# Optimization experiments

Hardware: AMD Instinct MI355X
Metric: run time of the kernel (lower is better)

## Reference

```python
import jax, jax.numpy as jnp
import numpy as np


def setup_inputs() -> dict:
    key = jax.random.key(0)
    ks = jax.random.split(key, 7)
    B, C, W, H = 4, 256, 128, 128
    s = 1.0 / np.sqrt(C)
    return {
        "x": jax.random.normal(ks[0], (B, C, W, H), dtype=jnp.float32),
        "wq": jax.random.normal(ks[1], (C, C), dtype=jnp.float32) * s,
        "bq": jax.random.normal(ks[2], (C,), dtype=jnp.float32) * s,
        "wk": jax.random.normal(ks[3], (C, C), dtype=jnp.float32) * s,
        "bk": jax.random.normal(ks[4], (C,), dtype=jnp.float32) * s,
        "wv": jax.random.normal(ks[5], (C, C), dtype=jnp.float32) * s,
        "bv": jax.random.normal(ks[6], (C,), dtype=jnp.float32) * s,
    }


def reference(x, wq, bq, wk, bk, wv, bv):
    B, C, W, H = x.shape
    N = W * H
    xf = x.reshape(B, C, N)  # flatten spatial: (B, C, N)
    # 1x1 convs are channel-mixing GEMMs: out[b,o,n] = sum_c w[o,c] x[b,c,n] + b[o]
    q = jnp.einsum('oc,bcn->bon', wq, xf) + bq[:, None]
    k = jnp.einsum('oc,bcn->bon', wk, xf) + bk[:, None]
    v = jnp.einsum('oc,bcn->bon', wv, xf) + bv[:, None]
    # channel-channel energy: (B, C, C)
    energy = jnp.einsum('bcn,bdn->bcd', q, k) / jnp.sqrt(jnp.float32(N))
    attention = jax.nn.softmax(energy, axis=-1)
    out = jnp.einsum('bcd,bdn->bcn', attention, v)
    return out.reshape(B, C, W, H) + x
```

## Files before the change

### kernel.cpp

```cpp
#include <hip/hip_runtime.h>
#include <stdint.h>

#define BB 4
#define CC 256
#define NN 16384
#define NSL 32

typedef unsigned short u16;
typedef __attribute__((ext_vector_type(8))) __bf16 bf16x8;
typedef __attribute__((ext_vector_type(4))) float f32x4;

__device__ __forceinline__ u16 f2bf(float f) {
  union { float f; uint32_t u; } c;
  c.f = f;
  uint32_t u = c.u;
  return (u16)((u + 0x7fffu + ((u >> 16) & 1u)) >> 16);
}

__device__ __forceinline__ void g2l16(const u16* g, u16* l) {
  __builtin_amdgcn_global_load_lds((__attribute__((address_space(1))) void*)g,
                                   (__attribute__((address_space(3))) void*)l, 16, 0, 0);
}

__device__ __forceinline__ void stage128x32(const u16* src, int stride, u16* lds, int tid) {
  int r = tid >> 2;
  int c = (tid & 3) << 3;
  g2l16(src + (size_t)r * stride + c, lds + r * 32 + c);
  g2l16(src + (size_t)(r + 64) * stride + c, lds + (r + 64) * 32 + c);
}

__device__ __forceinline__ void stage128x32_w8(const u16* src, int stride, u16* lds, int tid) {
  int r = tid >> 2;
  int c = (tid & 3) << 3;
  g2l16(src + (size_t)r * stride + c, lds + r * 32 + c);
}

__device__ __forceinline__ void stage256x32_w8(const u16* src, int stride, u16* lds, int tid) {
  int r = tid >> 2;
  int c = (tid & 3) << 3;
  g2l16(src + (size_t)r * stride + c, lds + r * 32 + c);
  g2l16(src + (size_t)(r + 128) * stride + c, lds + (r + 128) * 32 + c);
}

__device__ __forceinline__ void mfma_tile(const u16* As, const u16* Bs, int mb, int nb,
                                          int l16, int q8, f32x4 acc[4][4]) {
  bf16x8 af[4], bf[4];
#pragma unroll
  for (int i = 0; i < 4; i++) af[i] = *(const bf16x8*)&As[(mb + i * 16 + l16) * 32 + q8];
#pragma unroll
  for (int i = 0; i < 4; i++) bf[i] = *(const bf16x8*)&Bs[(nb + i * 16 + l16) * 32 + q8];
#pragma unroll
  for (int i = 0; i < 4; i++)
#pragma unroll
    for (int j = 0; j < 4; j++)
      acc[i][j] = __builtin_amdgcn_mfma_f32_16x16x32_bf16(af[i], bf[j], acc[i][j], 0, 0, 0);
}

__global__ __launch_bounds__(256) void prep_kernel(const float* __restrict__ x,
                                                   u16* __restrict__ xb,
                                                   u16* __restrict__ xbT,
                                                   float* __restrict__ s_part) {
  __shared__ float t[64][65];
  __shared__ float rs[64][4];
  int n0 = blockIdx.x * 64, c0 = blockIdx.y * 64, bz = blockIdx.z;
  int tid = threadIdx.x;
  int rr0 = tid >> 4, q4 = (tid & 15) * 4;
  const float* xs = x + ((size_t)bz * CC + c0) * NN + n0;
  u16* xbp = xb + ((size_t)bz * CC + c0) * NN + n0;
#pragma unroll
  for (int cc = rr0; cc < 64; cc += 16) {
    float4 v = *(const float4*)&xs[(size_t)cc * NN + q4];
    t[cc][q4] = v.x; t[cc][q4 + 1] = v.y; t[cc][q4 + 2] = v.z; t[cc][q4 + 3] = v.w;
    union { u16 h[4]; uint2 u; } pk;
    pk.h[0] = f2bf(v.x); pk.h[1] = f2bf(v.y); pk.h[2] = f2bf(v.z); pk.h[3] = f2bf(v.w);
    *(uint2*)&xbp[(size_t)cc * NN + q4] = pk.u;
  }
  __syncthreads();
  {
    int r = tid >> 2, q = tid & 3;
    float p = 0.f;
#pragma unroll
    for (int i = 0; i < 16; i++) p += t[r][q * 16 + i];
    rs[r][q] = p;
  }
  u16* od = xbT + ((size_t)bz * NN + n0) * CC + c0;
#pragma unroll
  for (int nn = rr0; nn < 64; nn += 16) {
    union { u16 h[4]; uint2 u; } pk;
    pk.h[0] = f2bf(t[q4][nn]); pk.h[1] = f2bf(t[q4 + 1][nn]);
    pk.h[2] = f2bf(t[q4 + 2][nn]); pk.h[3] = f2bf(t[q4 + 3][nn]);
    *(uint2*)&od[(size_t)nn * CC + q4] = pk.u;
  }
  __syncthreads();
  if (tid < 64)
    s_part[((size_t)bz * 256 + blockIdx.x) * CC + c0 + tid] =
        rs[tid][0] + rs[tid][1] + rs[tid][2] + rs[tid][3];
}

__global__ __launch_bounds__(256) void gram_kernel(const u16* __restrict__ xb,
                                                   float* __restrict__ Gp) {
  __shared__ u16 As[2][128 * 32], Bs[2][128 * 32];
  int tid = threadIdx.x;
  int c0 = (blockIdx.x >> 1) * 128, d0 = (blockIdx.x & 1) * 128;
  int sl = blockIdx.y, bz = blockIdx.z;
  const u16* A = xb + ((size_t)bz * CC + c0) * NN + sl * 512;
  const u16* Bt = xb + ((size_t)bz * CC + d0) * NN + sl * 512;
  f32x4 acc[4][4] = {};
  int wave = tid >> 6, lane = tid & 63;
  int mb = (wave >> 1) * 64, nb = (wave & 1) * 64;
  int quad = lane >> 4, l16 = lane & 15, q8 = quad * 8;
  for (int kk = 0; kk < 512; kk += 64) {
    stage128x32(A + kk, NN, As[0], tid);
    stage128x32(A + kk + 32, NN, As[1], tid);
    stage128x32(Bt + kk, NN, Bs[0], tid);
    stage128x32(Bt + kk + 32, NN, Bs[1], tid);
    __syncthreads();
    mfma_tile(As[0], Bs[0], mb, nb, l16, q8, acc);
    mfma_tile(As[1], Bs[1], mb, nb, l16, q8, acc);
    __syncthreads();
  }
  float* gp = Gp + ((size_t)sl * BB + bz) * CC * CC;
#pragma unroll
  for (int i = 0; i < 4; i++)
#pragma unroll
    for (int j = 0; j < 4; j++)
#pragma unroll
      for (int r = 0; r < 4; r++)
        gp[(size_t)(c0 + mb + i * 16 + quad * 4 + r) * CC + d0 + nb + j * 16 + l16] =
            acc[i][j][r];
}

__global__ __launch_bounds__(256) void reduce_kernel(const float* __restrict__ Gp,
                                                     const float* __restrict__ s_part,
                                                     const float* __restrict__ Wk,
                                                     float* __restrict__ G,
                                                     float* __restrict__ s,
                                                     float* __restrict__ WkT) {
  __shared__ float tw[32][33];
  int t = threadIdx.x, blk = blockIdx.x;
  size_t base = ((size_t)blk * 256 + t) * 4;
  float ax = 0.f, ay = 0.f, az = 0.f, aw = 0.f;
#pragma unroll 8
  for (int sl = 0; sl < NSL; sl++) {
    float4 v = *(const float4*)&Gp[(size_t)sl * (BB * CC * CC) + base];
    ax += v.x; ay += v.y; az += v.z; aw += v.w;
  }
  float4 o; o.x = ax; o.y = ay; o.z = az; o.w = aw;
  *(float4*)&G[base] = o;
  if (blk < BB) {
    float a = 0.f;
#pragma unroll 8
    for (int nt = 0; nt < 256; nt++) a += s_part[((size_t)blk * 256 + nt) * CC + t];
    s[blk * CC + t] = a;
  }
  if (blk < 64) {
    int tr = blk >> 3, tc = blk & 7;
    int r = t >> 5, c = t & 31;
#pragma unroll
    for (int i = 0; i < 4; i++)
      tw[r + i * 8][c] = Wk[(size_t)(tr * 32 + r + i * 8) * CC + tc * 32 + c];
    __syncthreads();
#pragma unroll
    for (int i = 0; i < 4; i++)
      WkT[(size_t)(tc * 32 + r + i * 8) * CC + tr * 32 + c] = tw[c][r + i * 8];
  }
}

__global__ __launch_bounds__(512) void mid_kernel(
    const float* __restrict__ G, const float* __restrict__ s,
    const float* __restrict__ Wq, const float* __restrict__ WkT,
    const float* __restrict__ Wv,
    const float* __restrict__ bq, const float* __restrict__ bk,
    const float* __restrict__ bv,
    u16* __restrict__ Mvb, float* __restrict__ bo) {
  __shared__ float sS[CC];
  __shared__ float wqS[4][CC];
  __shared__ float rS[4][CC];
  __shared__ float attS[4][CC];
  __shared__ float part[4][8][CC];
  __shared__ float redA[4][4], redB[4][4], redC[4][4], redD[4][4];
  int t = threadIdx.x;
  int o0 = blockIdx.x * 4, b = blockIdx.y;
  int wv = t >> 6, ln = t & 63;
  int col = t & 255;
  int row_a = t >> 8, row_b = row_a + 2;
  int c4 = ln << 2;
  int d0 = wv << 5;
  if (t < CC) sS[t] = s[b * CC + t];
  {
    const float* wqsrc = Wq + (size_t)o0 * CC;
    ((float*)wqS)[t] = wqsrc[t];
    ((float*)wqS)[t + 512] = wqsrc[t + 512];
  }
  __syncthreads();
  float pa = wqS[row_a][col] * sS[col];
  float pb = wqS[row_b][col] * sS[col];
#pragma unroll
  for (int d = 32; d > 0; d >>= 1) {
    pa += __shfl_xor(pa, d, 64);
    pb += __shfl_xor(pb, d, 64);
  }
  if (ln == 0) { redA[row_a][wv & 3] = pa; redA[row_b][wv & 3] = pb; }
  __syncthreads();
  float up_a = redA[row_a][0] + redA[row_a][1] + redA[row_a][2] + redA[row_a][3] +
               16384.f * bq[o0 + row_a];
  float up_b = redA[row_b][0] + redA[row_b][1] + redA[row_b][2] + redA[row_b][3] +
               16384.f * bq[o0 + row_b];
  const float* Gb = G + (size_t)b * CC * CC;
  {
    f32x4 va[4] = {};
    const float* gp = Gb + (size_t)d0 * CC + c4;
#pragma unroll 8
    for (int i = 0; i < 32; i++) {
      f32x4 g4 = *(const f32x4*)(gp + (size_t)i * CC);
      float w0 = wqS[0][d0 + i], w1 = wqS[1][d0 + i];
      float w2 = wqS[2][d0 + i], w3 = wqS[3][d0 + i];
      va[0] += g4 * w0; va[1] += g4 * w1; va[2] += g4 * w2; va[3] += g4 * w3;
    }
#pragma unroll
    for (int r = 0; r < 4; r++) *(f32x4*)&part[r][wv][c4] = va[r];
  }
  __syncthreads();
  {
    float r_a = bq[o0 + row_a] * sS[col];
    float r_b = bq[o0 + row_b] * sS[col];
#pragma unroll
    for (int w = 0; w < 8; w++) { r_a += part[row_a][w][col]; r_b += part[row_b][w][col]; }
    rS[row_a][col] = r_a;
    rS[row_b][col] = r_b;
  }
  __syncthreads();
  {
    f32x4 ve[4] = {};
    const float* wkp = WkT + (size_t)d0 * CC + c4;
#pragma unroll 8
    for (int i = 0; i < 32; i++) {
      f32x4 w4 = *(const f32x4*)(wkp + (size_t)i * CC);
      float r0 = rS[0][d0 + i], r1 = rS[1][d0 + i];
      float r2 = rS[2][d0 + i], r3 = rS[3][d0 + i];
      ve[0] += w4 * r0; ve[1] += w4 * r1; ve[2] += w4 * r2; ve[3] += w4 * r3;
    }
#pragma unroll
    for (int r = 0; r < 4; r++) *(f32x4*)&part[r][wv][c4] = ve[r];
  }
  __syncthreads();
  float bkc = bk[col];
  float e_a = up_a * bkc, e_b = up_b * bkc;
#pragma unroll
  for (int w = 0; w < 8; w++) { e_a += part[row_a][w][col]; e_b += part[row_b][w][col]; }
  e_a *= 0.0078125f;
  e_b *= 0.0078125f;
  float m_a = e_a, m_b = e_b;
#pragma unroll
  for (int d = 32; d > 0; d >>= 1) {
    m_a = fmaxf(m_a, __shfl_xor(m_a, d, 64));
    m_b = fmaxf(m_b, __shfl_xor(m_b, d, 64));
  }
  if (ln == 0) { redB[row_a][wv & 3] = m_a; redB[row_b][wv & 3] = m_b; }
  __syncthreads();
  m_a = fmaxf(fmaxf(redB[row_a][0], redB[row_a][1]), fmaxf(redB[row_a][2], redB[row_a][3]));
  m_b = fmaxf(fmaxf(redB[row_b][0], redB[row_b][1]), fmaxf(redB[row_b][2], redB[row_b][3]));
  e_a = __expf(e_a - m_a);
  e_b = __expf(e_b - m_b);
  float s_a = e_a, s_b = e_b;
#pragma unroll
  for (int d = 32; d > 0; d >>= 1) {
    s_a += __shfl_xor(s_a, d, 64);
    s_b += __shfl_xor(s_b, d, 64);
  }
  if (ln == 0) { redC[row_a][wv & 3] = s_a; redC[row_b][wv & 3] = s_b; }
  __syncthreads();
  float inv_a = 1.f / (redC[row_a][0] + redC[row_a][1] + redC[row_a][2] + redC[row_a][3]);
  float inv_b = 1.f / (redC[row_b][0] + redC[row_b][1] + redC[row_b][2] + redC[row_b][3]);
  float at_a = e_a * inv_a, at_b = e_b * inv_b;
  attS[row_a][col] = at_a;
  attS[row_b][col] = at_b;
  float bvc = bv[col];
  float ba = at_a * bvc, bb = at_b * bvc;
#pragma unroll
  for (int d = 32; d > 0; d >>= 1) {
    ba += __shfl_xor(ba, d, 64);
    bb += __shfl_xor(bb, d, 64);
  }
  if (ln == 0) { redD[row_a][wv & 3] = ba; redD[row_b][wv & 3] = bb; }
  __syncthreads();
  if (t < 4) bo[b * CC + o0 + t] = redD[t][0] + redD[t][1] + redD[t][2] + redD[t][3];
  {
    f32x4 vm[4] = {};
    const float* wp = Wv + (size_t)d0 * CC + c4;
#pragma unroll 8
    for (int i = 0; i < 32; i++) {
      f32x4 w4 = *(const f32x4*)(wp + (size_t)i * CC);
      float a0 = attS[0][d0 + i], a1 = attS[1][d0 + i];
      float a2 = attS[2][d0 + i], a3 = attS[3][d0 + i];
      vm[0] += w4 * a0; vm[1] += w4 * a1; vm[2] += w4 * a2; vm[3] += w4 * a3;
    }
#pragma unroll
    for (int r = 0; r < 4; r++) *(f32x4*)&part[r][wv][c4] = vm[r];
  }
  __syncthreads();
  float mv_a = 0.f, mv_b = 0.f;
#pragma unroll
  for (int w = 0; w < 8; w++) { mv_a += part[row_a][w][col]; mv_b += part[row_b][w][col]; }
  Mvb[((size_t)b * CC + o0 + row_a) * CC + col] = f2bf(mv_a);
  Mvb[((size_t)b * CC + o0 + row_b) * CC + col] = f2bf(mv_b);
}

__global__ __launch_bounds__(512) void out_kernel(const u16* __restrict__ Mvb,
                                                  const u16* __restrict__ xbT,
                                                  const float* __restrict__ bo,
                                                  const float* __restrict__ x,
                                                  float* __restrict__ out) {
  __shared__ union {
    struct { u16 As[2][128 * 32]; u16 Bs[2][256 * 32]; } st;
    float scr[8][64][20];
  } sm;
  int tid = threadIdx.x;
  int n0 = blockIdx.x * 256, m0 = blockIdx.y * 128, bz = blockIdx.z;
  const u16* A = Mvb + (size_t)bz * CC * CC + (size_t)m0 * CC;
  const u16* Bt = xbT + ((size_t)bz * NN + n0) * CC;
  f32x4 acc[4][4] = {};
  int wave = tid >> 6, lane = tid & 63;
  int mb = (wave & 1) * 64, nb = (wave >> 1) * 64;
  int quad = lane >> 4, l16 = lane & 15, q8 = quad * 8;
  for (int kk = 0; kk < CC; kk += 64) {
    stage128x32_w8(A + kk, CC, sm.st.As[0], tid);
    stage128x32_w8(A + kk + 32, CC, sm.st.As[1], tid);
    stage256x32_w8(Bt + kk, CC, sm.st.Bs[0], tid);
    stage256x32_w8(Bt + kk + 32, CC, sm.st.Bs[1], tid);
    __syncthreads();
    mfma_tile(sm.st.As[0], sm.st.Bs[0], mb, nb, l16, q8, acc);
    mfma_tile(sm.st.As[1], sm.st.Bs[1], mb, nb, l16, q8, acc);
    __syncthreads();
  }
  int l4 = lane >> 2;
  int cgl = lane & 3;
  float bc[4];
#pragma unroll
  for (int kq = 0; kq < 4; kq++) bc[kq] = bo[bz * CC + m0 + mb + kq * 16 + l4];
#pragma unroll
  for (int j = 0; j < 4; j++) {
#pragma unroll
    for (int i = 0; i < 4; i++)
#pragma unroll
      for (int r = 0; r < 4; r++)
        sm.scr[wave][i * 16 + quad * 4 + r][l16] = acc[i][j][r];
#pragma unroll
    for (int kq = 0; kq < 4; kq++) {
      int rloc = kq * 16 + l4;
      f32x4 v4 = *(const f32x4*)&sm.scr[wave][rloc][cgl * 4];
      int cg = m0 + mb + rloc;
      int ng = n0 + nb + j * 16 + cgl * 4;
      size_t idx = ((size_t)bz * CC + cg) * NN + ng;
      float4 xv = *(const float4*)&x[idx];
      float4 o4;
      o4.x = v4[0] + bc[kq] + xv.x;
      o4.y = v4[1] + bc[kq] + xv.y;
      o4.z = v4[2] + bc[kq] + xv.z;
      o4.w = v4[3] + bc[kq] + xv.w;
      *(float4*)&out[idx] = o4;
    }
  }
}

extern "C" void kernel_launch(void* const* d_in, const int* in_sizes, int n_in,
                              void* d_out, int out_size, void* d_ws, size_t ws_size,
                              hipStream_t stream) {
  (void)in_sizes; (void)n_in; (void)out_size; (void)ws_size;
  const float* x = (const float*)d_in[0];
  const float* wq = (const float*)d_in[1];
  const float* bq = (const float*)d_in[2];
  const float* wk = (const float*)d_in[3];
  const float* bk = (const float*)d_in[4];
  const float* wv = (const float*)d_in[5];
  const float* bv = (const float*)d_in[6];
  float* out = (float*)d_out;

  char* ws = (char*)d_ws;
  u16* xb      = (u16*)(ws + 0);
  u16* xbT     = (u16*)(ws + 33554432);
  float* Gp    = (float*)(ws + 67108864);
  float* G     = (float*)(ws + 100663296);
  float* s_prt = (float*)(ws + 101711872);
  float* s     = (float*)(ws + 102760448);
  u16* Mvb     = (u16*)(ws + 102764544);
  float* bo    = (float*)(ws + 103288832);
  float* WkT   = (float*)(ws + 103292928);

  prep_kernel<<<dim3(NN / 64, CC / 64, BB), 256, 0, stream>>>(x, xb, xbT, s_prt);
  gram_kernel<<<dim3(4, NSL, BB), 256, 0, stream>>>(xb, Gp);
  reduce_kernel<<<256, 256, 0, stream>>>(Gp, s_prt, wk, G, s, WkT);
  mid_kernel<<<dim3(CC / 4, BB), 512, 0, stream>>>(G, s, wq, WkT, wv, bq, bk, bv, Mvb, bo);
  out_kernel<<<dim3(NN / 256, CC / 128, BB), 512, 0, stream>>>(Mvb, xbT, bo, x, out);
}
```

Measured before the change: 218.9 us.

## Enlarge gram and output GEMM tiles to share staged operands across all channels

The gram kernel now stages one 256-row slice of xb per block and uses it as both MFMA operands. Each 512-thread block computes a 256x128 half of the Gram matrix, which cuts redundant global-to-LDS loads. The output GEMM block now covers all 256 output channels at once with a 4x8 accumulator tile per wave, so each xbT tile is loaded only once instead of twice. The cost is fewer blocks (lower parallelism), more registers per wave, and larger LDS use, which may reduce occupancy.

```diff
diff --git a/kernel.cpp b/kernel.cpp
--- a/kernel.cpp
+++ b/kernel.cpp
@@ -22,19 +22,6 @@
                                    (__attribute__((address_space(3))) void*)l, 16, 0, 0);
 }
 
-__device__ __forceinline__ void stage128x32(const u16* src, int stride, u16* lds, int tid) {
-  int r = tid >> 2;
-  int c = (tid & 3) << 3;
-  g2l16(src + (size_t)r * stride + c, lds + r * 32 + c);
-  g2l16(src + (size_t)(r + 64) * stride + c, lds + (r + 64) * 32 + c);
-}
-
-__device__ __forceinline__ void stage128x32_w8(const u16* src, int stride, u16* lds, int tid) {
-  int r = tid >> 2;
-  int c = (tid & 3) << 3;
-  g2l16(src + (size_t)r * stride + c, lds + r * 32 + c);
-}
-
 __device__ __forceinline__ void stage256x32_w8(const u16* src, int stride, u16* lds, int tid) {
   int r = tid >> 2;
   int c = (tid & 3) << 3;
@@ -53,6 +40,20 @@
   for (int i = 0; i < 4; i++)
 #pragma unroll
     for (int j = 0; j < 4; j++)
+      acc[i][j] = __builtin_amdgcn_mfma_f32_16x16x32_bf16(af[i], bf[j], acc[i][j], 0, 0, 0);
+}
+
+__device__ __forceinline__ void mfma_tile48(const u16* As, const u16* Bs, int mb, int nb,
+                                            int l16, int q8, f32x4 acc[4][8]) {
+  bf16x8 af[4], bf[8];
+#pragma unroll
+  for (int i = 0; i < 4; i++) af[i] = *(const bf16x8*)&As[(mb + i * 16 + l16) * 32 + q8];
+#pragma unroll
+  for (int j = 0; j < 8; j++) bf[j] = *(const bf16x8*)&Bs[(nb + j * 16 + l16) * 32 + q8];
+#pragma unroll
+  for (int i = 0; i < 4; i++)
+#pragma unroll
+    for (int j = 0; j < 8; j++)
       acc[i][j] = __builtin_amdgcn_mfma_f32_16x16x32_bf16(af[i], bf[j], acc[i][j], 0, 0, 0);
 }
 
@@ -97,26 +98,23 @@
         rs[tid][0] + rs[tid][1] + rs[tid][2] + rs[tid][3];
 }
 
-__global__ __launch_bounds__(256) void gram_kernel(const u16* __restrict__ xb,
+__global__ __launch_bounds__(512) void gram_kernel(const u16* __restrict__ xb,
                                                    float* __restrict__ Gp) {
-  __shared__ u16 As[2][128 * 32], Bs[2][128 * 32];
+  __shared__ u16 As[2][256 * 32];
   int tid = threadIdx.x;
-  int c0 = (blockIdx.x >> 1) * 128, d0 = (blockIdx.x & 1) * 128;
+  int d0 = blockIdx.x * 128;
   int sl = blockIdx.y, bz = blockIdx.z;
-  const u16* A = xb + ((size_t)bz * CC + c0) * NN + sl * 512;
-  const u16* Bt = xb + ((size_t)bz * CC + d0) * NN + sl * 512;
+  const u16* A = xb + (size_t)bz * CC * NN + sl * 512;
   f32x4 acc[4][4] = {};
   int wave = tid >> 6, lane = tid & 63;
-  int mb = (wave >> 1) * 64, nb = (wave & 1) * 64;
+  int mb = (wave & 3) * 64, nb = d0 + (wave >> 2) * 64;
   int quad = lane >> 4, l16 = lane & 15, q8 = quad * 8;
   for (int kk = 0; kk < 512; kk += 64) {
-    stage128x32(A + kk, NN, As[0], tid);
-    stage128x32(A + kk + 32, NN, As[1], tid);
-    stage128x32(Bt + kk, NN, Bs[0], tid);
-    stage128x32(Bt + kk + 32, NN, Bs[1], tid);
-    __syncthreads();
-    mfma_tile(As[0], Bs[0], mb, nb, l16, q8, acc);
-    mfma_tile(As[1], Bs[1], mb, nb, l16, q8, acc);
+    stage256x32_w8(A + kk, NN, As[0], tid);
+    stage256x32_w8(A + kk + 32, NN, As[1], tid);
+    __syncthreads();
+    mfma_tile(As[0], As[0], mb, nb, l16, q8, acc);
+    mfma_tile(As[1], As[1], mb, nb, l16, q8, acc);
     __syncthreads();
   }
   float* gp = Gp + ((size_t)sl * BB + bz) * CC * CC;
@@ -126,7 +124,7 @@
     for (int j = 0; j < 4; j++)
 #pragma unroll
       for (int r = 0; r < 4; r++)
-        gp[(size_t)(c0 + mb + i * 16 + quad * 4 + r) * CC + d0 + nb + j * 16 + l16] =
+        gp[(size_t)(mb + i * 16 + quad * 4 + r) * CC + nb + j * 16 + l16] =
             acc[i][j][r];
 }
 
@@ -312,34 +310,34 @@
                                                   const float* __restrict__ x,
                                                   float* __restrict__ out) {
   __shared__ union {
-    struct { u16 As[2][128 * 32]; u16 Bs[2][256 * 32]; } st;
+    struct { u16 As[2][256 * 32]; u16 Bs[2][256 * 32]; } st;
     float scr[8][64][20];
   } sm;
   int tid = threadIdx.x;
-  int n0 = blockIdx.x * 256, m0 = blockIdx.y * 128, bz = blockIdx.z;
-  const u16* A = Mvb + (size_t)bz * CC * CC + (size_t)m0 * CC;
+  int n0 = blockIdx.x * 256, bz = blockIdx.y;
+  const u16* A = Mvb + (size_t)bz * CC * CC;
   const u16* Bt = xbT + ((size_t)bz * NN + n0) * CC;
-  f32x4 acc[4][4] = {};
+  f32x4 acc[4][8] = {};
   int wave = tid >> 6, lane = tid & 63;
-  int mb = (wave & 1) * 64, nb = (wave >> 1) * 64;
+  int mb = (wave & 3) * 64, nb = (wave >> 2) * 128;
   int quad = lane >> 4, l16 = lane & 15, q8 = quad * 8;
   for (int kk = 0; kk < CC; kk += 64) {
-    stage128x32_w8(A + kk, CC, sm.st.As[0], tid);
-    stage128x32_w8(A + kk + 32, CC, sm.st.As[1], tid);
+    stage256x32_w8(A + kk, CC, sm.st.As[0], tid);
+    stage256x32_w8(A + kk + 32, CC, sm.st.As[1], tid);
     stage256x32_w8(Bt + kk, CC, sm.st.Bs[0], tid);
     stage256x32_w8(Bt + kk + 32, CC, sm.st.Bs[1], tid);
     __syncthreads();
-    mfma_tile(sm.st.As[0], sm.st.Bs[0], mb, nb, l16, q8, acc);
-    mfma_tile(sm.st.As[1], sm.st.Bs[1], mb, nb, l16, q8, acc);
+    mfma_tile48(sm.st.As[0], sm.st.Bs[0], mb, nb, l16, q8, acc);
+    mfma_tile48(sm.st.As[1], sm.st.Bs[1], mb, nb, l16, q8, acc);
     __syncthreads();
   }
   int l4 = lane >> 2;
   int cgl = lane & 3;
   float bc[4];
 #pragma unroll
-  for (int kq = 0; kq < 4; kq++) bc[kq] = bo[bz * CC + m0 + mb + kq * 16 + l4];
-#pragma unroll
-  for (int j = 0; j < 4; j++) {
+  for (int kq = 0; kq < 4; kq++) bc[kq] = bo[bz * CC + mb + kq * 16 + l4];
+#pragma unroll
+  for (int j = 0; j < 8; j++) {
 #pragma unroll
     for (int i = 0; i < 4; i++)
 #pragma unroll
@@ -349,7 +347,7 @@
     for (int kq = 0; kq < 4; kq++) {
       int rloc = kq * 16 + l4;
       f32x4 v4 = *(const f32x4*)&sm.scr[wave][rloc][cgl * 4];
-      int cg = m0 + mb + rloc;
+      int cg = mb + rloc;
       int ng = n0 + nb + j * 16 + cgl * 4;
       size_t idx = ((size_t)bz * CC + cg) * NN + ng;
       float4 xv = *(const float4*)&x[idx];
@@ -388,8 +386,8 @@
   float* WkT   = (float*)(ws + 103292928);
 
   prep_kernel<<<dim3(NN / 64, CC / 64, BB), 256, 0, stream>>>(x, xb, xbT, s_prt);
-  gram_kernel<<<dim3(4, NSL, BB), 256, 0, stream>>>(xb, Gp);
+  gram_kernel<<<dim3(2, NSL, BB), 512, 0, stream>>>(xb, Gp);
   reduce_kernel<<<256, 256, 0, stream>>>(Gp, s_prt, wk, G, s, WkT);
   mid_kernel<<<dim3(CC / 4, BB), 512, 0, stream>>>(G, s, wq, WkT, wv, bq, bk, bv, Mvb, bo);
-  out_kernel<<<dim3(NN / 256, CC / 128, BB), 512, 0, stream>>>(Mvb, xbT, bo, x, out);
-}
+  out_kernel<<<dim3(NN / 256, BB), 512, 0, stream>>>(Mvb, xbT, bo, x, out);
+}
```

Result: slower. 224.2 us (+2.5%).
